# Optimization experiments

Measured on AMD Instinct MI355X. Metric: run time of the kernel, lower is better.

Reference implementation:

```python
import jax, jax.numpy as jnp
import numpy as np

B, N, D2, S = 64, 4096, 128, 512  # b, n, 2*d, size_s


def setup_inputs() -> dict:
    key = jax.random.key(0)
    k1, k2, k3, k4 = jax.random.split(key, 4)
    s_past = jax.random.randint(k1, (B, N), 0, S)
    yq = jax.random.normal(k2, (B, 1, D2), dtype=jnp.float32)
    y_past = jax.random.normal(k3, (B, N, D2), dtype=jnp.float32)
    w_mat = jax.random.normal(k4, (D2, D2), dtype=jnp.float32)
    return {"s_past": s_past, "yq": yq, "y_past": y_past, "w_mat": w_mat, "size_s": S}


def reference(s_past, yq, y_past, w_mat, size_s):
    # attn_logits[b,n] = yq[b,0,:] @ w_mat @ y_past[b,n,:]
    attn_logits = jnp.einsum('bqd,de,bne->bn', yq, w_mat, y_past)
    attn = jax.nn.softmax(attn_logits, axis=-1)  # (b, n)
    b, n = s_past.shape
    # post_est[b, s] = sum_n attn[b, n] * [s_past[b, n] == s]
    # fused scatter-add instead of materializing one-hot (b, n, S)
    flat_ids = (s_past + size_s * jnp.arange(b, dtype=s_past.dtype)[:, None]).reshape(-1)
    post_est = jax.ops.segment_sum(attn.reshape(-1), flat_ids,
                                   num_segments=b * size_s).reshape(b, size_s)
    return post_est
```

## Files before the change

### kernel.cpp

```cpp
#include <hip/hip_runtime.h>
#include <math.h>

#define BB 64
#define NN 4096
#define DD 128
#define SS 512
#define CHUNKS 16
#define RPC 256
#define SUBT 4

__global__ __launch_bounds__(256) void fused_kernel(
    const float* __restrict__ y_past, const float* __restrict__ yq,
    const float* __restrict__ w, const int* __restrict__ s_past,
    float* __restrict__ bins_g, float* __restrict__ pmax) {
    int b = blockIdx.x, chunk = blockIdx.y;
    int t = threadIdx.x;

    __shared__ float4 ytile[64 * 33];
    __shared__ float syq[DD];
    __shared__ float qsh[DD];
    __shared__ float bins[SS];
    __shared__ int   ssh[RPC];
    __shared__ float wred[8];

    if (t < DD) syq[t] = yq[b * DD + t];
    bins[t] = 0.f;
    bins[t + 256] = 0.f;
    ssh[t] = s_past[b * NN + chunk * RPC + t];
    __syncthreads();

    if (t < DD) {
        float acc = 0.f;
#pragma unroll
        for (int d = 0; d < DD; ++d) acc = fmaf(syq[d], w[d * DD + t], acc);
        qsh[t] = acc;
    }
    __syncthreads();

    int j = t & 3;
    int r = t >> 2;
    float4 qreg[8];
#pragma unroll
    for (int k = 0; k < 8; ++k) qreg[k] = ((const float4*)qsh)[j * 8 + k];

    const float4* gp =
        (const float4*)y_past + ((size_t)b * NN + (size_t)chunk * RPC) * 32;

    float pv[SUBT];
#pragma unroll
    for (int s = 0; s < SUBT; ++s) {
#pragma unroll
        for (int k = 0; k < 8; ++k) {
            int idx = t + k * 256;
            int rr = idx >> 5, cc = idx & 31;
            ytile[rr * 33 + cc] = gp[s * 2048 + idx];
        }
        __syncthreads();

        float4 acc = {0.f, 0.f, 0.f, 0.f};
#pragma unroll
        for (int k = 0; k < 8; ++k) {
            float4 yv = ytile[r * 33 + j * 8 + k];
            acc.x = fmaf(qreg[k].x, yv.x, acc.x);
            acc.y = fmaf(qreg[k].y, yv.y, acc.y);
            acc.z = fmaf(qreg[k].z, yv.z, acc.z);
            acc.w = fmaf(qreg[k].w, yv.w, acc.w);
        }
        float p = (acc.x + acc.y) + (acc.z + acc.w);
        p += __shfl_xor(p, 1, 64);
        p += __shfl_xor(p, 2, 64);
        pv[s] = p;
        __syncthreads();
    }

    float m = fmaxf(fmaxf(pv[0], pv[1]), fmaxf(pv[2], pv[3]));
#pragma unroll
    for (int off = 32; off > 0; off >>= 1) m = fmaxf(m, __shfl_xor(m, off, 64));
    int wave = t >> 6, lane = t & 63;
    if (lane == 0) wred[wave] = m;
    __syncthreads();
    m = fmaxf(fmaxf(wred[0], wred[1]), fmaxf(wred[2], wred[3]));

    if (j == 0) {
#pragma unroll
        for (int s = 0; s < SUBT; ++s)
            atomicAdd(&bins[ssh[s * 64 + r]], __expf(pv[s] - m));
    }
    __syncthreads();

    float* bg = bins_g + ((size_t)b * CHUNKS + chunk) * SS;
    bg[t] = bins[t];
    bg[t + 256] = bins[t + 256];
    if (t == 0) pmax[b * CHUNKS + chunk] = m;
}

__global__ __launch_bounds__(512) void combine_kernel(
    const float* __restrict__ bins_g, const float* __restrict__ pmax,
    float* __restrict__ out) {
    int b = blockIdx.x;
    int t = threadIdx.x;
    __shared__ float scale[CHUNKS];
    __shared__ float red[8];
    __shared__ float sInv;

    if (t < CHUNKS) scale[t] = pmax[b * CHUNKS + t];
    __syncthreads();
    if (t == 0) {
        float M = scale[0];
#pragma unroll
        for (int c = 1; c < CHUNKS; ++c) M = fmaxf(M, scale[c]);
#pragma unroll
        for (int c = 0; c < CHUNKS; ++c) scale[c] = __expf(scale[c] - M);
    }
    __syncthreads();

    float acc = 0.f;
#pragma unroll
    for (int c = 0; c < CHUNKS; ++c)
        acc = fmaf(bins_g[((size_t)b * CHUNKS + c) * SS + t], scale[c], acc);

    float s = acc;
#pragma unroll
    for (int off = 32; off > 0; off >>= 1) s += __shfl_xor(s, off, 64);
    if ((t & 63) == 0) red[t >> 6] = s;
    __syncthreads();
    if (t == 0) {
        float S = 0.f;
#pragma unroll
        for (int i = 0; i < 8; ++i) S += red[i];
        sInv = 1.f / S;
    }
    __syncthreads();

    out[b * SS + t] = acc * sInv;
}

extern "C" void kernel_launch(void* const* d_in, const int* in_sizes, int n_in,
                              void* d_out, int out_size, void* d_ws, size_t ws_size,
                              hipStream_t stream) {
    const int*   s_past = (const int*)d_in[0];
    const float* yq     = (const float*)d_in[1];
    const float* y_past = (const float*)d_in[2];
    const float* w_mat  = (const float*)d_in[3];

    float* ws     = (float*)d_ws;
    float* bins_g = ws;
    float* pmax   = bins_g + BB * CHUNKS * SS;
    float* out    = (float*)d_out;

    fused_kernel<<<dim3(BB, CHUNKS), 256, 0, stream>>>(y_past, yq, w_mat,
                                                       s_past, bins_g, pmax);
    combine_kernel<<<BB, SS, 0, stream>>>(bins_g, pmax, out);
}
```

Baseline: 204.9 us.

## Split q precompute into own kernel and read y_past directly from global

Moves the yq@W projection into a separate small kernel so each fused block no longer recomputes q. It drops the shared-memory staging of y_past in favour of direct float4 loads, with 8 lanes per row reduced by shuffles. It also doubles the chunk count to 32 with 128 rows per block to raise parallelism. The costs are an extra kernel launch and twice as many partial bin buffers for the combine kernel to read.

```diff
diff --git a/kernel.cpp b/kernel.cpp
--- a/kernel.cpp
+++ b/kernel.cpp
@@ -5,93 +5,104 @@
 #define NN 4096
 #define DD 128
 #define SS 512
-#define CHUNKS 16
-#define RPC 256
-#define SUBT 4
+#define CH2 32
+#define RPC2 128
+
+__global__ void compute_q_kernel(const float* __restrict__ yq,
+                                 const float* __restrict__ w,
+                                 float* __restrict__ q) {
+    int b = blockIdx.x;
+    int e = threadIdx.x;
+    __shared__ float syq[DD];
+    syq[e] = yq[b * DD + e];
+    __syncthreads();
+    float acc = 0.f;
+#pragma unroll
+    for (int d = 0; d < DD; ++d) acc = fmaf(syq[d], w[d * DD + e], acc);
+    q[b * DD + e] = acc;
+}
 
 __global__ __launch_bounds__(256) void fused_kernel(
-    const float* __restrict__ y_past, const float* __restrict__ yq,
-    const float* __restrict__ w, const int* __restrict__ s_past,
-    float* __restrict__ bins_g, float* __restrict__ pmax) {
+    const float* __restrict__ y_past, const float* __restrict__ q,
+    const int* __restrict__ s_past, float* __restrict__ bins_g,
+    float* __restrict__ pmax) {
     int b = blockIdx.x, chunk = blockIdx.y;
     int t = threadIdx.x;
 
-    __shared__ float4 ytile[64 * 33];
-    __shared__ float syq[DD];
+    __shared__ float bins[SS];
     __shared__ float qsh[DD];
-    __shared__ float bins[SS];
-    __shared__ int   ssh[RPC];
-    __shared__ float wred[8];
+    __shared__ int ssh[RPC2];
+    __shared__ float wred[4];
+    __shared__ float s_m;
 
-    if (t < DD) syq[t] = yq[b * DD + t];
     bins[t] = 0.f;
     bins[t + 256] = 0.f;
-    ssh[t] = s_past[b * NN + chunk * RPC + t];
+    if (t < DD) qsh[t] = q[b * DD + t];
+    if (t < RPC2) ssh[t] = s_past[b * NN + chunk * RPC2 + t];
     __syncthreads();
 
-    if (t < DD) {
+    int g = t & 7;
+    int rg = t >> 3;
+
+    float4 qreg[4];
+#pragma unroll
+    for (int k = 0; k < 4; ++k) qreg[k] = ((const float4*)qsh)[g + 8 * k];
+
+    const float4* gp =
+        (const float4*)y_past + ((size_t)b * NN + (size_t)chunk * RPC2) * 32;
+
+    float pv[4];
+#pragma unroll
+    for (int s = 0; s < 4; ++s) {
+        int row = s * 32 + rg;
+        const float4* rp = gp + (size_t)row * 32 + g;
+        float4 a0 = rp[0], a1 = rp[8], a2 = rp[16], a3 = rp[24];
         float acc = 0.f;
+        acc = fmaf(qreg[0].x, a0.x, acc);
+        acc = fmaf(qreg[0].y, a0.y, acc);
+        acc = fmaf(qreg[0].z, a0.z, acc);
+        acc = fmaf(qreg[0].w, a0.w, acc);
+        acc = fmaf(qreg[1].x, a1.x, acc);
+        acc = fmaf(qreg[1].y, a1.y, acc);
+        acc = fmaf(qreg[1].z, a1.z, acc);
+        acc = fmaf(qreg[1].w, a1.w, acc);
+        acc = fmaf(qreg[2].x, a2.x, acc);
+        acc = fmaf(qreg[2].y, a2.y, acc);
+        acc = fmaf(qreg[2].z, a2.z, acc);
+        acc = fmaf(qreg[2].w, a2.w, acc);
+        acc = fmaf(qreg[3].x, a3.x, acc);
+        acc = fmaf(qreg[3].y, a3.y, acc);
+        acc = fmaf(qreg[3].z, a3.z, acc);
+        acc = fmaf(qreg[3].w, a3.w, acc);
+        acc += __shfl_xor(acc, 1, 64);
+        acc += __shfl_xor(acc, 2, 64);
+        acc += __shfl_xor(acc, 4, 64);
+        pv[s] = acc;
+    }
+
+    float m = fmaxf(fmaxf(pv[0], pv[1]), fmaxf(pv[2], pv[3]));
+    m = fmaxf(m, __shfl_xor(m, 8, 64));
+    m = fmaxf(m, __shfl_xor(m, 16, 64));
+    m = fmaxf(m, __shfl_xor(m, 32, 64));
+    int wave = t >> 6, lane = t & 63;
+    if (lane == 0) wred[wave] = m;
+    __syncthreads();
+    if (t == 0)
+        s_m = fmaxf(fmaxf(wred[0], wred[1]), fmaxf(wred[2], wred[3]));
+    __syncthreads();
+    m = s_m;
+
+    if (g == 0) {
 #pragma unroll
-        for (int d = 0; d < DD; ++d) acc = fmaf(syq[d], w[d * DD + t], acc);
-        qsh[t] = acc;
+        for (int s = 0; s < 4; ++s)
+            atomicAdd(&bins[ssh[s * 32 + rg]], __expf(pv[s] - m));
     }
     __syncthreads();
 
-    int j = t & 3;
-    int r = t >> 2;
-    float4 qreg[8];
-#pragma unroll
-    for (int k = 0; k < 8; ++k) qreg[k] = ((const float4*)qsh)[j * 8 + k];
-
-    const float4* gp =
-        (const float4*)y_past + ((size_t)b * NN + (size_t)chunk * RPC) * 32;
-
-    float pv[SUBT];
-#pragma unroll
-    for (int s = 0; s < SUBT; ++s) {
-#pragma unroll
-        for (int k = 0; k < 8; ++k) {
-            int idx = t + k * 256;
-            int rr = idx >> 5, cc = idx & 31;
-            ytile[rr * 33 + cc] = gp[s * 2048 + idx];
-        }
-        __syncthreads();
-
-        float4 acc = {0.f, 0.f, 0.f, 0.f};
-#pragma unroll
-        for (int k = 0; k < 8; ++k) {
-            float4 yv = ytile[r * 33 + j * 8 + k];
-            acc.x = fmaf(qreg[k].x, yv.x, acc.x);
-            acc.y = fmaf(qreg[k].y, yv.y, acc.y);
-            acc.z = fmaf(qreg[k].z, yv.z, acc.z);
-            acc.w = fmaf(qreg[k].w, yv.w, acc.w);
-        }
-        float p = (acc.x + acc.y) + (acc.z + acc.w);
-        p += __shfl_xor(p, 1, 64);
-        p += __shfl_xor(p, 2, 64);
-        pv[s] = p;
-        __syncthreads();
-    }
-
-    float m = fmaxf(fmaxf(pv[0], pv[1]), fmaxf(pv[2], pv[3]));
-#pragma unroll
-    for (int off = 32; off > 0; off >>= 1) m = fmaxf(m, __shfl_xor(m, off, 64));
-    int wave = t >> 6, lane = t & 63;
-    if (lane == 0) wred[wave] = m;
-    __syncthreads();
-    m = fmaxf(fmaxf(wred[0], wred[1]), fmaxf(wred[2], wred[3]));
-
-    if (j == 0) {
-#pragma unroll
-        for (int s = 0; s < SUBT; ++s)
-            atomicAdd(&bins[ssh[s * 64 + r]], __expf(pv[s] - m));
-    }
-    __syncthreads();
-
-    float* bg = bins_g + ((size_t)b * CHUNKS + chunk) * SS;
+    float* bg = bins_g + ((size_t)b * CH2 + chunk) * SS;
     bg[t] = bins[t];
     bg[t + 256] = bins[t + 256];
-    if (t == 0) pmax[b * CHUNKS + chunk] = m;
+    if (t == 0) pmax[b * CH2 + chunk] = m;
 }
 
 __global__ __launch_bounds__(512) void combine_kernel(
@@ -99,25 +110,25 @@
     float* __restrict__ out) {
     int b = blockIdx.x;
     int t = threadIdx.x;
-    __shared__ float scale[CHUNKS];
+    __shared__ float scale[CH2];
     __shared__ float red[8];
     __shared__ float sInv;
 
-    if (t < CHUNKS) scale[t] = pmax[b * CHUNKS + t];
+    if (t < CH2) scale[t] = pmax[b * CH2 + t];
     __syncthreads();
     if (t == 0) {
         float M = scale[0];
 #pragma unroll
-        for (int c = 1; c < CHUNKS; ++c) M = fmaxf(M, scale[c]);
+        for (int c = 1; c < CH2; ++c) M = fmaxf(M, scale[c]);
 #pragma unroll
-        for (int c = 0; c < CHUNKS; ++c) scale[c] = __expf(scale[c] - M);
+        for (int c = 0; c < CH2; ++c) scale[c] = __expf(scale[c] - M);
     }
     __syncthreads();
 
     float acc = 0.f;
 #pragma unroll
-    for (int c = 0; c < CHUNKS; ++c)
-        acc = fmaf(bins_g[((size_t)b * CHUNKS + c) * SS + t], scale[c], acc);
+    for (int c = 0; c < CH2; ++c)
+        acc = fmaf(bins_g[((size_t)b * CH2 + c) * SS + t], scale[c], acc);
 
     float s = acc;
 #pragma unroll
@@ -144,11 +155,13 @@
     const float* w_mat  = (const float*)d_in[3];
 
     float* ws     = (float*)d_ws;
-    float* bins_g = ws;
-    float* pmax   = bins_g + BB * CHUNKS * SS;
+    float* q      = ws;
+    float* bins_g = q + BB * DD;
+    float* pmax   = bins_g + BB * CH2 * SS;
     float* out    = (float*)d_out;
 
-    fused_kernel<<<dim3(BB, CHUNKS), 256, 0, stream>>>(y_past, yq, w_mat,
-                                                       s_past, bins_g, pmax);
+    compute_q_kernel<<<BB, DD, 0, stream>>>(yq, w_mat, q);
+    fused_kernel<<<dim3(BB, CH2), 256, 0, stream>>>(y_past, q, s_past, bins_g,
+                                                    pmax);
     combine_kernel<<<BB, SS, 0, stream>>>(bins_g, pmax, out);
 }
```

Result: no change. 207.2 us (+1.1%).
